# Kernel optimization log

Hardware: AMD Instinct MI355X
Metric: run time of the kernel (lower is better)

The kernel has to match this reference:

```python
import jax, jax.numpy as jnp
import numpy as np

POOLED_SIZES = [12, 16, 20, 24]
NUM_HEADS = 8
EPS_LN = 1e-5


def _pool_mat(in_size, out_size):
    # torch adaptive_avg_pool1d/2d semantics as an averaging matrix [out, in]
    m = np.zeros((out_size, in_size), np.float32)
    for i in range(out_size):
        s = (i * in_size) // out_size
        e = -((-(i + 1) * in_size) // out_size)  # ceil
        m[i, s:e] = 1.0 / (e - s)
    return jnp.asarray(m)


def _dwconv(x, w, b):
    # depthwise 3x3, stride 1, padding 1 (NCHW, OIHW with I=1)
    y = jax.lax.conv_general_dilated(
        x, w, (1, 1), 'SAME', feature_group_count=x.shape[1],
        dimension_numbers=('NCHW', 'OIHW', 'NCHW'))
    return y + b[None, :, None, None]


def _ln(x, g, b):
    m = x.mean(-1, keepdims=True)
    v = jnp.mean((x - m) ** 2, axis=-1, keepdims=True)
    return (x - m) / jnp.sqrt(v + EPS_LN) * g + b


def setup_inputs() -> dict:
    key = jax.random.key(0)
    ks = jax.random.split(key, 16)
    B, H, W, C = 4, 56, 56, 256
    hid = 4 * C
    nrm = lambda k, shape, s=0.02: jax.random.normal(k, shape, jnp.float32) * s
    inp = {
        'x': jax.random.normal(ks[0], (B, H * W, C), jnp.float32),
        'cpe_w': nrm(ks[1], (C, 1, 3, 3)), 'cpe_b': jnp.zeros((C,), jnp.float32),
        'norm1_w': jnp.ones((C,), jnp.float32), 'norm1_b': jnp.zeros((C,), jnp.float32),
        'q_w': nrm(ks[2], (C, C)),
        'kv_w': nrm(ks[3], (2 * C, C)),
        'attn_norm_w': jnp.ones((C,), jnp.float32), 'attn_norm_b': jnp.zeros((C,), jnp.float32),
        'proj_w': nrm(ks[4], (C, C)), 'proj_b': jnp.zeros((C,), jnp.float32),
        'norm2_w': jnp.ones((C,), jnp.float32), 'norm2_b': jnp.zeros((C,), jnp.float32),
        'fc1_w': nrm(ks[5], (hid, C)), 'fc1_b': jnp.zeros((hid,), jnp.float32),
        'irb_conv_w': nrm(ks[6], (hid, 1, 3, 3)), 'irb_conv_b': jnp.zeros((hid,), jnp.float32),
        'fc2_w': nrm(ks[7], (C, hid)), 'fc2_b': jnp.zeros((C,), jnp.float32),
        'H': H, 'W': W,
    }
    for i in range(4):
        inp[f'dconv{i}_w'] = nrm(ks[8 + i], (C, 1, 3, 3))
        inp[f'dconv{i}_b'] = jnp.zeros((C,), jnp.float32)
    return inp


def _forward(x, cpe_w, cpe_b, norm1_w, norm1_b, q_w, kv_w, attn_norm_w, attn_norm_b,
             proj_w, proj_b, dconv0_w, dconv0_b, dconv1_w, dconv1_b, dconv2_w, dconv2_b,
             dconv3_w, dconv3_b, norm2_w, norm2_b, fc1_w, fc1_b, irb_conv_w, irb_conv_b,
             fc2_w, fc2_b, H, W):
    B, N, C = x.shape
    nh = NUM_HEADS
    hd = C // nh
    scale = hd ** -0.5
    # conditional positional encoding: x = cpe(x) + x
    xi = x.transpose(0, 2, 1).reshape(B, C, H, W)
    xi = _dwconv(xi, cpe_w, cpe_b) + xi
    x = xi.reshape(B, C, N).transpose(0, 2, 1)
    # ---- pyramid pooling attention ----
    xn = _ln(x, norm1_w, norm1_b)
    q = (xn @ q_w.T).reshape(B, N, nh, hd).transpose(0, 2, 1, 3)  # [B,nh,N,hd]
    x_ = xn.transpose(0, 2, 1).reshape(B, C, H, W)
    dws = [(dconv0_w, dconv0_b), (dconv1_w, dconv1_b),
           (dconv2_w, dconv2_b), (dconv3_w, dconv3_b)]
    pools = []
    for p, (dw, db) in zip(POOLED_SIZES, dws):
        ph = _pool_mat(H, p)
        pw = _pool_mat(W, p)
        pool = jnp.einsum('oi,bcij,pj->bcop', ph, x_, pw)  # adaptive avg pool (p,p)
        pool = pool + _dwconv(pool, dw, db)
        pools.append(pool.reshape(B, C, -1))
    pools = jnp.concatenate(pools, axis=2).transpose(0, 2, 1)  # [B,P,C], P=1376
    pools = _ln(pools, attn_norm_w, attn_norm_b)
    kv = (pools @ kv_w.T).reshape(B, -1, 2, nh, hd).transpose(2, 0, 3, 1, 4)
    k, v = kv[0], kv[1]  # [B,nh,P,hd]
    attn = jax.nn.softmax(jnp.einsum('bhnd,bhpd->bhnp', q, k) * scale, axis=-1)
    out = jnp.einsum('bhnp,bhpd->bhnd', attn, v).transpose(0, 2, 1, 3).reshape(B, N, C)
    out = out @ proj_w.T + proj_b
    x = x + out
    # ---- IRB FFN ----
    xn = _ln(x, norm2_w, norm2_b)
    xi = xn.transpose(0, 2, 1).reshape(B, C, H, W)
    h = jnp.einsum('oc,bchw->bohw', fc1_w, xi) + fc1_b[None, :, None, None]
    h = jax.nn.gelu(h, approximate=False)
    h = h + _dwconv(h, irb_conv_w, irb_conv_b)
    o = jnp.einsum('oc,bchw->bohw', fc2_w, h) + fc2_b[None, :, None, None]
    x = x + o.reshape(B, C, N).transpose(0, 2, 1)
    return x


def reference(x, cpe_w, cpe_b, norm1_w, norm1_b, q_w, kv_w, attn_norm_w, attn_norm_b,
              proj_w, proj_b, dconv0_w, dconv0_b, dconv1_w, dconv1_b, dconv2_w, dconv2_b,
              dconv3_w, dconv3_b, norm2_w, norm2_b, fc1_w, fc1_b, irb_conv_w, irb_conv_b,
              fc2_w, fc2_b, H, W):
    return _forward(x, cpe_w, cpe_b, norm1_w, norm1_b, q_w, kv_w, attn_norm_w, attn_norm_b,
                    proj_w, proj_b, dconv0_w, dconv0_b, dconv1_w, dconv1_b, dconv2_w, dconv2_b,
                    dconv3_w, dconv3_b, norm2_w, norm2_b, fc1_w, fc1_b, irb_conv_w, irb_conv_b,
                    fc2_w, fc2_b, H, W)
```

## Files before the change

kernel.cpp:

```cpp
#include <hip/hip_runtime.h>
#include <hip/hip_bf16.h>

#define BQ 4
#define HH 56
#define WW 56
#define NN (HH*WW)
#define CC 256
#define NHEAD 8
#define HD 32
#define PP 1376
#define PPAD 1408
#define HIDN 1024
#define EPS_LN 1e-5f
#define QSCALE_LOG2E 0.25503484f

typedef unsigned short bf16u;
typedef __attribute__((ext_vector_type(8))) short short8;
typedef __attribute__((ext_vector_type(4))) float f32x4;

__device__ __forceinline__ float bf2f(bf16u u){
  union { unsigned int i; float f; } v; v.i = ((unsigned int)u) << 16; return v.f;
}
__device__ __forceinline__ bf16u f2bf(float f){
  unsigned int x = __float_as_uint(f);
  x += 0x7fffu + ((x >> 16) & 1u);
  return (bf16u)(x >> 16);
}
__device__ __forceinline__ bf16u f2bf_r(float f){
  return (bf16u)((__float_as_uint(f) + 0x8000u) >> 16);
}
__device__ __forceinline__ void cvt4(const ushort4 u, float* d){
  d[0]=bf2f(u.x); d[1]=bf2f(u.y); d[2]=bf2f(u.z); d[3]=bf2f(u.w);
}

#define CSEG 4
__global__ void k_init(const float* __restrict__ qw, const float* __restrict__ kvw,
                       const float* __restrict__ pw, const float* __restrict__ f1,
                       const float* __restrict__ f2, bf16u* __restrict__ wo,
                       const float* __restrict__ x, const float* __restrict__ w,
                       const float* __restrict__ bias, const float* __restrict__ g,
                       const float* __restrict__ be, float* __restrict__ x1,
                       bf16u* __restrict__ xnb){
  if (blockIdx.x < 768){
    int off = (blockIdx.x*256 + threadIdx.x) * 4;
    const float* s;
    if (off < 65536)       s = qw  + off;
    else if (off < 196608) s = kvw + off - 65536;
    else if (off < 262144) s = pw  + off - 196608;
    else if (off < 524288) s = f1  + off - 262144;
    else                   s = f2  + off - 524288;
    float4 v = *(const float4*)s;
    ushort4 u = {f2bf(v.x), f2bf(v.y), f2bf(v.z), f2bf(v.w)};
    *(ushort4*)(wo + off) = u;
    return;
  }
  int t = threadIdx.x;
  int wave = t >> 6, lane = t & 63;
  int widx = (blockIdx.x - 768)*4 + wave;
  const int nseg = WW/CSEG;
  int xseg = widx % nseg;
  int y    = (widx / nseg) % HH;
  int b    = widx / (nseg*HH);
  int c0 = lane*4;
  int x0 = xseg*CSEG;
  float wv[36];
  {
    const float* wp = w + (size_t)c0*9;
#pragma unroll
    for (int i = 0; i < 9; i++){
      float4 v = *(const float4*)(wp + i*4);
      wv[i*4+0]=v.x; wv[i*4+1]=v.y; wv[i*4+2]=v.z; wv[i*4+3]=v.w;
    }
  }
  float4 bi4 = *(const float4*)&bias[c0];
  float bi[4] = {bi4.x, bi4.y, bi4.z, bi4.w};
  float4 gv = *(const float4*)&g[c0];
  float4 bv = *(const float4*)&be[c0];
  const float* rowc = x + ((size_t)b*NN + (size_t)y*WW)*CC + c0;
  const float* rowm = (y > 0)    ? rowc - (size_t)WW*CC : rowc;
  const float* rowp = (y < HH-1) ? rowc + (size_t)WW*CC : rowc;
  if (y == 0){
#pragma unroll
    for (int cc = 0; cc < 4; cc++){ wv[cc*9+0]=0.f; wv[cc*9+1]=0.f; wv[cc*9+2]=0.f; }
  }
  if (y == HH-1){
#pragma unroll
    for (int cc = 0; cc < 4; cc++){ wv[cc*9+6]=0.f; wv[cc*9+7]=0.f; wv[cc*9+8]=0.f; }
  }
  float win[3][3][4];
  float4 rawA[3], rawB[3];
  if (x0 == 0){
#pragma unroll
    for (int r = 0; r < 3; r++)
#pragma unroll
      for (int cc = 0; cc < 4; cc++) win[0][r][cc] = 0.f;
  } else {
    size_t o = (size_t)(x0-1)*CC;
    float4 a0 = *(const float4*)&rowm[o];
    float4 a1 = *(const float4*)&rowc[o];
    float4 a2 = *(const float4*)&rowp[o];
    win[0][0][0]=a0.x; win[0][0][1]=a0.y; win[0][0][2]=a0.z; win[0][0][3]=a0.w;
    win[0][1][0]=a1.x; win[0][1][1]=a1.y; win[0][1][2]=a1.z; win[0][1][3]=a1.w;
    win[0][2][0]=a2.x; win[0][2][1]=a2.y; win[0][2][2]=a2.z; win[0][2][3]=a2.w;
  }
  {
    size_t o = (size_t)x0*CC;
    float4 a0 = *(const float4*)&rowm[o];
    float4 a1 = *(const float4*)&rowc[o];
    float4 a2 = *(const float4*)&rowp[o];
    win[1][0][0]=a0.x; win[1][0][1]=a0.y; win[1][0][2]=a0.z; win[1][0][3]=a0.w;
    win[1][1][0]=a1.x; win[1][1][1]=a1.y; win[1][1][2]=a1.z; win[1][1][3]=a1.w;
    win[1][2][0]=a2.x; win[1][2][1]=a2.y; win[1][2][2]=a2.z; win[1][2][3]=a2.w;
  }
  {
    size_t o = (size_t)(x0+1)*CC;
    rawA[0] = *(const float4*)&rowm[o];
    rawA[1] = *(const float4*)&rowc[o];
    rawA[2] = *(const float4*)&rowp[o];
  }
#pragma unroll
  for (int xx = 0; xx < CSEG; xx++){
    float4* cur = (xx & 1) ? rawB : rawA;
    float4* nxt = (xx & 1) ? rawA : rawB;
    if (xx < CSEG-1){
      int xg = x0 + xx + 2;
      if (xg < WW){
        size_t o = (size_t)xg*CC;
        nxt[0] = *(const float4*)&rowm[o];
        nxt[1] = *(const float4*)&rowc[o];
        nxt[2] = *(const float4*)&rowp[o];
      } else {
        float4 z = {0.f,0.f,0.f,0.f};
        nxt[0] = z; nxt[1] = z; nxt[2] = z;
      }
    }
    int sl2 = (xx+2)%3, slm = xx%3, slc = (xx+1)%3;
#pragma unroll
    for (int r = 0; r < 3; r++){
      win[sl2][r][0]=cur[r].x; win[sl2][r][1]=cur[r].y;
      win[sl2][r][2]=cur[r].z; win[sl2][r][3]=cur[r].w;
    }
    float o4[4];
#pragma unroll
    for (int cc = 0; cc < 4; cc++){
      float a = bi[cc];
      a += win[slm][0][cc]*wv[cc*9+0] + win[slc][0][cc]*wv[cc*9+1] + win[sl2][0][cc]*wv[cc*9+2];
      a += win[slm][1][cc]*wv[cc*9+3] + win[slc][1][cc]*wv[cc*9+4] + win[sl2][1][cc]*wv[cc*9+5];
      a += win[slm][2][cc]*wv[cc*9+6] + win[slc][2][cc]*wv[cc*9+7] + win[sl2][2][cc]*wv[cc*9+8];
      o4[cc] = win[slc][1][cc] + a;
    }
    size_t pix = (size_t)b*NN + (size_t)y*WW + x0 + xx;
    float4 ov = {o4[0],o4[1],o4[2],o4[3]};
    *(float4*)&x1[pix*CC + c0] = ov;
    float s  = o4[0]+o4[1]+o4[2]+o4[3];
    float s2 = o4[0]*o4[0]+o4[1]*o4[1]+o4[2]*o4[2]+o4[3]*o4[3];
#pragma unroll
    for (int off = 32; off; off >>= 1){
      s  += __shfl_xor(s,  off);
      s2 += __shfl_xor(s2, off);
    }
    float mean = s * (1.f/CC);
    float var  = s2 * (1.f/CC) - mean*mean;
    float rstd = rsqrtf(var + EPS_LN);
    float y0 = (o4[0]-mean)*rstd*gv.x + bv.x;
    float y1 = (o4[1]-mean)*rstd*gv.y + bv.y;
    float y2 = (o4[2]-mean)*rstd*gv.z + bv.z;
    float y3 = (o4[3]-mean)*rstd*gv.w + bv.w;
    ushort4 yb = {f2bf_r(y0), f2bf_r(y1), f2bf_r(y2), f2bf_r(y3)};
    *(ushort4*)&xnb[pix*CC + c0] = yb;
  }
}

__global__ void k_ln_bf16(const float* __restrict__ X, const float* __restrict__ g,
                          const float* __restrict__ be, bf16u* __restrict__ Y){
  int row = blockIdx.x;
  int t = threadIdx.x;
  float v = X[(size_t)row*CC + t];
  float s = v, s2 = v*v;
#pragma unroll
  for (int off = 32; off; off >>= 1){
    s  += __shfl_down(s,  off);
    s2 += __shfl_down(s2, off);
  }
  __shared__ float red[10];
  int wv_ = t >> 6, ln = t & 63;
  if (ln == 0){ red[wv_] = s; red[4+wv_] = s2; }
  __syncthreads();
  if (t == 0){
    float S  = red[0]+red[1]+red[2]+red[3];
    float S2 = red[4]+red[5]+red[6]+red[7];
    float mean = S * (1.f/CC);
    float var  = S2 * (1.f/CC) - mean*mean;
    red[8] = mean; red[9] = rsqrtf(var + EPS_LN);
  }
  __syncthreads();
  float mean = red[8], rstd = red[9];
  Y[(size_t)row*CC + t] = f2bf_r((v - mean) * rstd * g[t] + be[t]);
}

__global__ void k_pool(const bf16u* __restrict__ xnb, float* __restrict__ praw){
  int bp = blockIdx.x;
  int b = bp / PP, p = bp % PP;
  int ps, pi;
  if (p < 144)      { ps = 12; pi = p; }
  else if (p < 400) { ps = 16; pi = p - 144; }
  else if (p < 800) { ps = 20; pi = p - 400; }
  else              { ps = 24; pi = p - 800; }
  int oi = pi / ps, oj = pi % ps;
  int si = oi*HH/ps, ei = ((oi+1)*HH + ps - 1)/ps;
  int sj = oj*WW/ps, ej = ((oj+1)*WW + ps - 1)/ps;
  int c = threadIdx.x;
  const bf16u* xb = xnb + (size_t)b*NN*CC + c;
  float acc = 0.f;
  for (int i = si; i < ei; i++)
    for (int j = sj; j < ej; j++)
      acc += bf2f(xb[(size_t)(i*WW+j)*CC]);
  praw[(size_t)bp*CC + c] = acc / (float)((ei-si)*(ej-sj));
}

__global__ void k_pooldw_ln(const float* __restrict__ praw,
    const float* w0, const float* b0, const float* w1, const float* b1,
    const float* w2, const float* b2, const float* w3, const float* b3,
    const float* __restrict__ g, const float* __restrict__ be,
    bf16u* __restrict__ pools){
  int bp = blockIdx.x;
  int b = bp / PP, p = bp % PP;
  int ps, pi, off; const float *w, *bi;
  if (p < 144)      { ps=12; pi=p;     off=0;   w=w0; bi=b0; }
  else if (p < 400) { ps=16; pi=p-144; off=144; w=w1; bi=b1; }
  else if (p < 800) { ps=20; pi=p-400; off=400; w=w2; bi=b2; }
  else              { ps=24; pi=p-800; off=800; w=w3; bi=b3; }
  int oi = pi/ps, oj = pi%ps;
  int c = threadIdx.x;
  const float* base = praw + (size_t)(b*PP + off)*CC + c;
  float acc = bi[c];
#pragma unroll
  for (int kh = 0; kh < 3; kh++){
    int ii = oi + kh - 1; if (ii < 0 || ii >= ps) continue;
#pragma unroll
    for (int kw = 0; kw < 3; kw++){
      int jj = oj + kw - 1; if (jj < 0 || jj >= ps) continue;
      acc += base[(size_t)(ii*ps+jj)*CC] * w[c*9 + kh*3 + kw];
    }
  }
  float v = base[(size_t)(oi*ps+oj)*CC] + acc;
  float s = v, s2 = v*v;
#pragma unroll
  for (int o2_ = 32; o2_; o2_ >>= 1){
    s  += __shfl_down(s,  o2_);
    s2 += __shfl_down(s2, o2_);
  }
  __shared__ float red[10];
  int wv_ = c >> 6, ln = c & 63;
  if (ln == 0){ red[wv_] = s; red[4+wv_] = s2; }
  __syncthreads();
  if (c == 0){
    float S  = red[0]+red[1]+red[2]+red[3];
    float S2 = red[4]+red[5]+red[6]+red[7];
    float mean = S * (1.f/CC);
    float var  = S2 * (1.f/CC) - mean*mean;
    red[8] = mean; red[9] = rsqrtf(var + EPS_LN);
  }
  __syncthreads();
  float mean = red[8], rstd = red[9];
  pools[(size_t)bp*CC + c] = f2bf_r((v - mean) * rstd * g[c] + be[c]);
}

#define GST 40
template<int MT, int NT, bool OUT_BF16, bool HAS_BIAS, bool DO_GELU, bool HAS_RES, bool VT_OUT>
__global__ __launch_bounds__(256) void k_gemm_mfma(const bf16u* __restrict__ A,
                       const bf16u* __restrict__ Wt,
                       const float* __restrict__ bias, void* Outp,
                       const float* Res, bf16u* __restrict__ vtout,
                       int M, int Nout, int K, float oscale){
  constexpr int MW = (MT == 128) ? 4 : 2;
  constexpr int NW = (NT == 128) ? 4 : 2;
  __shared__ bf16u Ash[2][MT*GST];
  __shared__ bf16u Bsh[2][NT*GST];
  int t = threadIdx.x;
  int wave = t >> 6, lane = t & 63, quad = lane >> 4, l16 = lane & 15;
  int m0 = blockIdx.y * MT, n0 = blockIdx.x * NT;
  int wm = (wave >> 1) * (MT/2);
  int wn = (wave & 1) * (NT/2);
  int ar = (MT==128) ? (t>>1) : (t>>2);
  int ac = (MT==128) ? ((t&1)*16) : ((t&3)*8);
  int br = (NT==128) ? (t>>1) : (t>>2);
  int bc = (NT==128) ? ((t&1)*16) : ((t&3)*8);
  int astore = ar*GST + ac;
  int bstore = br*GST + bc;
  const bf16u* ap = A  + (size_t)(m0+ar)*K + ac;
  const bf16u* bp = Wt + (size_t)(n0+br)*K + bc;

  uint4 a0 = *(const uint4*)ap, a1;
  uint4 b0 = *(const uint4*)bp, b1;
  if constexpr (MT == 128) a1 = *(const uint4*)(ap+8);
  if constexpr (NT == 128) b1 = *(const uint4*)(bp+8);
  *(uint4*)&Ash[0][astore] = a0;
  if constexpr (MT == 128) *(uint4*)&Ash[0][astore + 8] = a1;
  *(uint4*)&Bsh[0][bstore] = b0;
  if constexpr (NT == 128) *(uint4*)&Bsh[0][bstore + 8] = b1;
  ap += 32; bp += 32;
  a0 = *(const uint4*)ap;
  if constexpr (MT == 128) a1 = *(const uint4*)(ap+8);
  b0 = *(const uint4*)bp;
  if constexpr (NT == 128) b1 = *(const uint4*)(bp+8);
  __syncthreads();

  f32x4 zero = {0.f,0.f,0.f,0.f};
  f32x4 acc[MW][NW];
#pragma unroll
  for (int i = 0; i < MW; i++)
#pragma unroll
    for (int j = 0; j < NW; j++) acc[i][j] = zero;

  int nks = K >> 5;
  for (int ks = 0; ks < nks; ks++){
    int cur = ks & 1;
    if (ks < nks-1){
      *(uint4*)&Ash[cur^1][astore] = a0;
      if constexpr (MT == 128) *(uint4*)&Ash[cur^1][astore + 8] = a1;
      *(uint4*)&Bsh[cur^1][bstore] = b0;
      if constexpr (NT == 128) *(uint4*)&Bsh[cur^1][bstore + 8] = b1;
      if (ks < nks-2){
        ap += 32; bp += 32;
        a0 = *(const uint4*)ap;
        if constexpr (MT == 128) a1 = *(const uint4*)(ap+8);
        b0 = *(const uint4*)bp;
        if constexpr (NT == 128) b1 = *(const uint4*)(bp+8);
      }
    }
    short8 af[MW], bfr[NW];
#pragma unroll
    for (int mi = 0; mi < MW; mi++)
      af[mi] = *(const short8*)&Ash[cur][(wm + mi*16 + l16)*GST + quad*8];
#pragma unroll
    for (int ni = 0; ni < NW; ni++)
      bfr[ni] = *(const short8*)&Bsh[cur][(wn + ni*16 + l16)*GST + quad*8];
#pragma unroll
    for (int mi = 0; mi < MW; mi++)
#pragma unroll
      for (int ni = 0; ni < NW; ni++)
        acc[mi][ni] = __builtin_amdgcn_mfma_f32_16x16x32_bf16(af[mi], bfr[ni], acc[mi][ni], 0,0,0);
    if (ks < nks-1) __syncthreads();
  }
#pragma unroll
  for (int mi = 0; mi < MW; mi++){
#pragma unroll
    for (int r = 0; r < 4; r++){
      int row = m0 + wm + mi*16 + quad*4 + r;
#pragma unroll
      for (int ni = 0; ni < NW; ni++){
        int col = n0 + wn + ni*16 + l16;
        float v = acc[mi][ni][r] * oscale;
        if constexpr (HAS_BIAS) v += bias[col];
        if constexpr (DO_GELU)  v = 0.5f*v*(1.f + erff(v*0.70710678118654752f));
        if constexpr (HAS_RES)  v += Res[(size_t)row*Nout + col];
        if constexpr (VT_OUT){
          if (col < CC){
            ((bf16u*)Outp)[(size_t)row*Nout + col] = f2bf_r(v);
          } else {
            int bb = row / PP, pp = row - bb*PP;
            vtout[((size_t)(bb*CC + (col - CC)))*PPAD + pp] = f2bf_r(v);
          }
        } else if constexpr (OUT_BF16){
          ((bf16u*)Outp)[(size_t)row*Nout + col] = f2bf_r(v);
        } else {
          ((float*)Outp)[(size_t)row*Nout + col] = v;
        }
      }
    }
  }
}

#define KST 40
#define VST 72
__global__ __launch_bounds__(256) void k_attn_mfma(const bf16u* __restrict__ q,
                       const bf16u* __restrict__ kvb, const bf16u* __restrict__ vt,
                       bf16u* __restrict__ out){
  __shared__ bf16u Ksh[2][64*KST];
  __shared__ bf16u Vsh[2][32*VST];
  int t = threadIdx.x;
  int wave = t >> 6, lane = t & 63, quad = lane >> 4, l16 = lane & 15;
  int bid = blockIdx.x;
  int qt = bid % (NN/64);
  int h  = (bid / (NN/64)) % NHEAD;
  int b  = bid / ((NN/64)*NHEAD);
  int q0 = qt*64 + wave*16;
  const bf16u* qptr = q + (size_t)(b*NN + q0 + l16)*CC + h*HD + quad*8;
  short8 qf = *(const short8*)qptr;
  f32x4 zero = {0.f,0.f,0.f,0.f};
  f32x4 o0 = zero, o1 = zero;
  float ls = 0.f;
  int ksr = t >> 2, ksc = (t & 3) * 8;
  int vsr = t >> 3, vsc = (t & 7) * 8;
  const bf16u* ksrc = kvb + (size_t)(b*PP + ksr)*(2*CC) + h*HD + ksc;
  const bf16u* vsrc = vt  + (size_t)(b*CC + h*HD + vsr)*PPAD + vsc;
  int krow = (ksr & 32) | ((ksr & 4) << 2) | ((ksr & 24) >> 1) | (ksr & 3);
  int kstore = krow*KST + ksc;
  int vstore = vsr*VST + vsc;
  int koffA = l16*KST + quad*8;
  int koffB = koffA + 16*KST;
  int voff0 = l16*VST + quad*8;
  int voff1 = (16 + l16)*VST + quad*8;

  uint4 kreg = *(const uint4*)ksrc;
  uint4 vreg = *(const uint4*)vsrc;
  *(uint4*)&Ksh[0][kstore] = kreg;
  *(uint4*)&Vsh[0][vstore] = vreg;
  ksrc += (size_t)64*(2*CC); vsrc += 64;
  kreg = *(const uint4*)ksrc; vreg = *(const uint4*)vsrc;
  __syncthreads();

#define PAIR(KB, VB, cb) { \
    short8 kfa = *(const short8*)&KB[cb*KST + koffA]; \
    short8 kfb = *(const short8*)&KB[cb*KST + koffB]; \
    f32x4 sa = __builtin_amdgcn_mfma_f32_16x16x32_bf16(kfa, qf, zero, 0,0,0); \
    f32x4 sb = __builtin_amdgcn_mfma_f32_16x16x32_bf16(kfb, qf, zero, 0,0,0); \
    float ea0 = __builtin_amdgcn_exp2f(sa[0]), ea1 = __builtin_amdgcn_exp2f(sa[1]); \
    float ea2 = __builtin_amdgcn_exp2f(sa[2]), ea3 = __builtin_amdgcn_exp2f(sa[3]); \
    float eb0 = __builtin_amdgcn_exp2f(sb[0]), eb1 = __builtin_amdgcn_exp2f(sb[1]); \
    float eb2 = __builtin_amdgcn_exp2f(sb[2]), eb3 = __builtin_amdgcn_exp2f(sb[3]); \
    ls += ((ea0+ea1)+(ea2+ea3)) + ((eb0+eb1)+(eb2+eb3)); \
    short8 pa; \
    pa[0]=(short)f2bf_r(ea0); pa[1]=(short)f2bf_r(ea1); \
    pa[2]=(short)f2bf_r(ea2); pa[3]=(short)f2bf_r(ea3); \
    pa[4]=(short)f2bf_r(eb0); pa[5]=(short)f2bf_r(eb1); \
    pa[6]=(short)f2bf_r(eb2); pa[7]=(short)f2bf_r(eb3); \
    short8 vf0 = *(const short8*)&VB[cb + voff0]; \
    short8 vf1 = *(const short8*)&VB[cb + voff1]; \
    o0 = __builtin_amdgcn_mfma_f32_16x16x32_bf16(pa, vf0, o0, 0,0,0); \
    o1 = __builtin_amdgcn_mfma_f32_16x16x32_bf16(pa, vf1, o1, 0,0,0); }

  for (int ch = 0; ch < PPAD/64 - 1; ch++){
    int cur = ch & 1;
    bf16u* KB = &Ksh[cur][0];
    bf16u* VB = &Vsh[cur][0];
    *(uint4*)&Ksh[cur^1][kstore] = kreg;
    *(uint4*)&Vsh[cur^1][vstore] = vreg;
    if (ch < PPAD/64 - 2){
      ksrc += (size_t)64*(2*CC); vsrc += 64;
      kreg = *(const uint4*)ksrc; vreg = *(const uint4*)vsrc;
    }
    PAIR(KB, VB, 0)
    PAIR(KB, VB, 32)
    __syncthreads();
  }
  {
    bf16u* KB = &Ksh[1][0];
    bf16u* VB = &Vsh[1][0];
    PAIR(KB, VB, 0)
  }
#undef PAIR

  ls += __shfl_xor(ls, 16); ls += __shfl_xor(ls, 32);
#pragma unroll
  for (int r = 0; r < 4; r++){
    int qq = quad*4 + r;
    float inv = 1.f / __shfl(ls, qq);
    size_t base = (size_t)(b*NN + q0 + qq)*CC + h*HD;
    out[base + l16]      = f2bf_r(o0[r]*inv);
    out[base + 16 + l16] = f2bf_r(o1[r]*inv);
  }
}

#define DWSEG 8
__global__ __launch_bounds__(256) void k_dwh(const bf16u* __restrict__ h, const float* __restrict__ w,
                      const float* __restrict__ bias, bf16u* __restrict__ h2){
  const int nseg = WW/DWSEG;
  int bid = blockIdx.x;
  int xseg = bid % nseg;
  int y    = (bid / nseg) % HH;
  int b    = bid / (nseg*HH);
  int t = threadIdx.x;
  int c0 = t*4;
  int x0 = xseg*DWSEG;
  float wv[36];
  {
    const float4* wp = (const float4*)(w + (size_t)c0*9);
#pragma unroll
    for (int i = 0; i < 9; i++){
      float4 v = wp[i];
      wv[i*4+0]=v.x; wv[i*4+1]=v.y; wv[i*4+2]=v.z; wv[i*4+3]=v.w;
    }
  }
  float4 bi4 = *(const float4*)&bias[c0];
  float bi[4] = {bi4.x, bi4.y, bi4.z, bi4.w};
  const bf16u* rowc = h + ((size_t)b*NN + (size_t)y*WW)*HIDN + c0;
  const bf16u* rowm = (y > 0)    ? rowc - (size_t)WW*HIDN : rowc;
  const bf16u* rowp = (y < HH-1) ? rowc + (size_t)WW*HIDN : rowc;
  if (y == 0){
#pragma unroll
    for (int cc = 0; cc < 4; cc++){ wv[cc*9+0]=0.f; wv[cc*9+1]=0.f; wv[cc*9+2]=0.f; }
  }
  if (y == HH-1){
#pragma unroll
    for (int cc = 0; cc < 4; cc++){ wv[cc*9+6]=0.f; wv[cc*9+7]=0.f; wv[cc*9+8]=0.f; }
  }
  float win[3][3][4];
  ushort4 rawA[3], rawB[3];
  if (x0 == 0){
#pragma unroll
    for (int r = 0; r < 3; r++)
#pragma unroll
      for (int cc = 0; cc < 4; cc++) win[0][r][cc] = 0.f;
  } else {
    size_t o = (size_t)(x0-1)*HIDN;
    ushort4 a0 = *(const ushort4*)&rowm[o];
    ushort4 a1 = *(const ushort4*)&rowc[o];
    ushort4 a2 = *(const ushort4*)&rowp[o];
    cvt4(a0, win[0][0]); cvt4(a1, win[0][1]); cvt4(a2, win[0][2]);
  }
  {
    size_t o = (size_t)x0*HIDN;
    ushort4 a0 = *(const ushort4*)&rowm[o];
    ushort4 a1 = *(const ushort4*)&rowc[o];
    ushort4 a2 = *(const ushort4*)&rowp[o];
    cvt4(a0, win[1][0]); cvt4(a1, win[1][1]); cvt4(a2, win[1][2]);
  }
  {
    size_t o = (size_t)(x0+1)*HIDN;
    rawA[0] = *(const ushort4*)&rowm[o];
    rawA[1] = *(const ushort4*)&rowc[o];
    rawA[2] = *(const ushort4*)&rowp[o];
  }
#pragma unroll
  for (int x = 0; x < DWSEG; x++){
    ushort4* cur = (x & 1) ? rawB : rawA;
    ushort4* nxt = (x & 1) ? rawA : rawB;
    if (x < DWSEG-1){
      int xg = x0 + x + 2;
      if (xg < WW){
        size_t o = (size_t)xg*HIDN;
        nxt[0] = *(const ushort4*)&rowm[o];
        nxt[1] = *(const ushort4*)&rowc[o];
        nxt[2] = *(const ushort4*)&rowp[o];
      } else {
        ushort4 z = {0,0,0,0};
        nxt[0] = z; nxt[1] = z; nxt[2] = z;
      }
    }
    int s2 = (x+2)%3, sm = x%3, sc_ = (x+1)%3;
    cvt4(cur[0], win[s2][0]); cvt4(cur[1], win[s2][1]); cvt4(cur[2], win[s2][2]);
    float o0[4];
#pragma unroll
    for (int cc = 0; cc < 4; cc++){
      float a = bi[cc];
      a += win[sm][0][cc]*wv[cc*9+0] + win[sc_][0][cc]*wv[cc*9+1] + win[s2][0][cc]*wv[cc*9+2];
      a += win[sm][1][cc]*wv[cc*9+3] + win[sc_][1][cc]*wv[cc*9+4] + win[s2][1][cc]*wv[cc*9+5];
      a += win[sm][2][cc]*wv[cc*9+6] + win[sc_][2][cc]*wv[cc*9+7] + win[s2][2][cc]*wv[cc*9+8];
      o0[cc] = win[sc_][1][cc] + a;
    }
    ushort4 ou = {f2bf_r(o0[0]), f2bf_r(o0[1]), f2bf_r(o0[2]), f2bf_r(o0[3])};
    *(ushort4*)&h2[((size_t)b*NN + (size_t)y*WW + x0 + x)*HIDN + c0] = ou;
  }
}

extern "C" void kernel_launch(void* const* d_in, const int* in_sizes, int n_in,
                              void* d_out, int out_size, void* d_ws, size_t ws_size,
                              hipStream_t stream){
  const float* x      = (const float*)d_in[0];
  const float* cpe_w  = (const float*)d_in[1];
  const float* cpe_b  = (const float*)d_in[2];
  const float* n1w    = (const float*)d_in[3];
  const float* n1b    = (const float*)d_in[4];
  const float* q_w    = (const float*)d_in[5];
  const float* kv_w   = (const float*)d_in[6];
  const float* anw    = (const float*)d_in[7];
  const float* anb    = (const float*)d_in[8];
  const float* proj_w = (const float*)d_in[9];
  const float* proj_b = (const float*)d_in[10];
  const float* n2w    = (const float*)d_in[11];
  const float* n2b    = (const float*)d_in[12];
  const float* fc1_w  = (const float*)d_in[13];
  const float* fc1_b  = (const float*)d_in[14];
  const float* irb_w  = (const float*)d_in[15];
  const float* irb_b  = (const float*)d_in[16];
  const float* fc2_w  = (const float*)d_in[17];
  const float* fc2_b  = (const float*)d_in[18];
  const float* dw0    = (const float*)d_in[21];
  const float* db0    = (const float*)d_in[22];
  const float* dw1    = (const float*)d_in[23];
  const float* db1    = (const float*)d_in[24];
  const float* dw2    = (const float*)d_in[25];
  const float* db2    = (const float*)d_in[26];
  const float* dw3    = (const float*)d_in[27];
  const float* db3    = (const float*)d_in[28];

  const size_t BNC = (size_t)BQ*NN*CC;
  const size_t BPC = (size_t)BQ*PP*CC;
  const size_t BNH = (size_t)BQ*NN*HIDN;

  float* x1   = (float*)d_ws;
  bf16u* xnb  = (bf16u*)(x1 + BNC);
  bf16u* wbuf = xnb + BNC;
  bf16u* wq   = wbuf;
  bf16u* wkv  = wbuf + 65536;
  bf16u* wpj  = wbuf + 196608;
  bf16u* wf1  = wbuf + 262144;
  bf16u* wf2  = wbuf + 524288;
  float* A0   = (float*)(wbuf + 786432);
  bf16u* qb   = (bf16u*)A0;
  float* praw = (float*)(qb + BNC);
  bf16u* poolsb = (bf16u*)(praw + BPC);
  bf16u* kvb  = poolsb + BPC;
  bf16u* vtb  = kvb + (size_t)BQ*PP*2*CC;
  bf16u* hbuf = (bf16u*)A0;
  bf16u* h2buf = hbuf + BNH;

  k_init<<<768 + (BQ*HH*(WW/CSEG))/4, 256, 0, stream>>>(q_w, kv_w, proj_w, fc1_w, fc2_w, wbuf,
                                            x, cpe_w, cpe_b, n1w, n1b, x1, xnb);
  k_gemm_mfma<64,64,true,false,false,false,false><<<dim3(CC/64, BQ*NN/64), 256, 0, stream>>>(
      xnb, wq, nullptr, qb, nullptr, nullptr, BQ*NN, CC, CC, QSCALE_LOG2E);
  k_pool<<<BQ*PP, 256, 0, stream>>>(xnb, praw);
  k_pooldw_ln<<<BQ*PP, 256, 0, stream>>>(praw, dw0,db0, dw1,db1, dw2,db2, dw3,db3,
                                         anw, anb, poolsb);
  k_gemm_mfma<64,64,true,false,false,false,true><<<dim3(2*CC/64, BQ*PP/64), 256, 0, stream>>>(
      poolsb, wkv, nullptr, kvb, nullptr, vtb, BQ*PP, 2*CC, CC, 1.0f);
  k_attn_mfma<<<BQ*NHEAD*(NN/64), 256, 0, stream>>>(qb, kvb, vtb, qb);
  k_gemm_mfma<64,64,false,true,false,true,false><<<dim3(CC/64, BQ*NN/64), 256, 0, stream>>>(
      qb, wpj, proj_b, x1, x1, nullptr, BQ*NN, CC, CC, 1.0f);
  k_ln_bf16<<<BQ*NN, 256, 0, stream>>>(x1, n2w, n2b, xnb);
  k_gemm_mfma<128,128,true,true,true,false,false><<<dim3(HIDN/128, BQ*NN/128), 256, 0, stream>>>(
      xnb, wf1, fc1_b, hbuf, nullptr, nullptr, BQ*NN, HIDN, CC, 1.0f);
  k_dwh<<<BQ*HH*(WW/DWSEG), 256, 0, stream>>>(hbuf, irb_w, irb_b, h2buf);
  k_gemm_mfma<64,64,false,true,false,true,false><<<dim3(CC/64, BQ*NN/64), 256, 0, stream>>>(
      h2buf, wf2, fc2_b, d_out, x1, nullptr, BQ*NN, CC, HIDN, 1.0f);
}
```

Baseline: 311.1 us.

## Deepen GEMM global prefetch, compute softmax sum via MFMA, warp-per-row LayerNorm

The GEMM main loop is unrolled by two and keeps two register sets of global prefetch, so loads are issued two K-steps ahead of use. In attention, the softmax denominator is now taken from an extra MFMA against a ones vector, which sums the bf16-rounded probabilities, and probabilities are packed with byte-perm instead of per-element conversion. The second LayerNorm now handles one row per wave using float4 loads and needs no shared-memory reduction or barriers. These changes cost more registers in the GEMM and one more MFMA per chunk in attention, and the normaliser now uses rounded rather than full-precision probabilities.

```diff
diff --git a/kernel.cpp b/kernel.cpp
--- a/kernel.cpp
+++ b/kernel.cpp
@@ -173,29 +173,27 @@
 
 __global__ void k_ln_bf16(const float* __restrict__ X, const float* __restrict__ g,
                           const float* __restrict__ be, bf16u* __restrict__ Y){
-  int row = blockIdx.x;
-  int t = threadIdx.x;
-  float v = X[(size_t)row*CC + t];
-  float s = v, s2 = v*v;
+  int wave = threadIdx.x >> 6, lane = threadIdx.x & 63;
+  int row = blockIdx.x*4 + wave;
+  int c0 = lane*4;
+  float4 v = *(const float4*)&X[(size_t)row*CC + c0];
+  float s  = v.x+v.y+v.z+v.w;
+  float s2 = v.x*v.x+v.y*v.y+v.z*v.z+v.w*v.w;
 #pragma unroll
   for (int off = 32; off; off >>= 1){
-    s  += __shfl_down(s,  off);
-    s2 += __shfl_down(s2, off);
-  }
-  __shared__ float red[10];
-  int wv_ = t >> 6, ln = t & 63;
-  if (ln == 0){ red[wv_] = s; red[4+wv_] = s2; }
-  __syncthreads();
-  if (t == 0){
-    float S  = red[0]+red[1]+red[2]+red[3];
-    float S2 = red[4]+red[5]+red[6]+red[7];
-    float mean = S * (1.f/CC);
-    float var  = S2 * (1.f/CC) - mean*mean;
-    red[8] = mean; red[9] = rsqrtf(var + EPS_LN);
-  }
-  __syncthreads();
-  float mean = red[8], rstd = red[9];
-  Y[(size_t)row*CC + t] = f2bf_r((v - mean) * rstd * g[t] + be[t]);
+    s  += __shfl_xor(s,  off);
+    s2 += __shfl_xor(s2, off);
+  }
+  float mean = s * (1.f/CC);
+  float var  = s2 * (1.f/CC) - mean*mean;
+  float rstd = rsqrtf(var + EPS_LN);
+  float4 gv = *(const float4*)&g[c0];
+  float4 bv = *(const float4*)&be[c0];
+  ushort4 yb = {f2bf_r((v.x-mean)*rstd*gv.x + bv.x),
+                f2bf_r((v.y-mean)*rstd*gv.y + bv.y),
+                f2bf_r((v.z-mean)*rstd*gv.z + bv.z),
+                f2bf_r((v.w-mean)*rstd*gv.w + bv.w)};
+  *(ushort4*)&Y[(size_t)row*CC + c0] = yb;
 }
 
 __global__ void k_pool(const bf16u* __restrict__ xnb, float* __restrict__ praw){
@@ -291,19 +289,27 @@
   const bf16u* ap = A  + (size_t)(m0+ar)*K + ac;
   const bf16u* bp = Wt + (size_t)(n0+br)*K + bc;
 
-  uint4 a0 = *(const uint4*)ap, a1;
-  uint4 b0 = *(const uint4*)bp, b1;
-  if constexpr (MT == 128) a1 = *(const uint4*)(ap+8);
-  if constexpr (NT == 128) b1 = *(const uint4*)(bp+8);
-  *(uint4*)&Ash[0][astore] = a0;
-  if constexpr (MT == 128) *(uint4*)&Ash[0][astore + 8] = a1;
-  *(uint4*)&Bsh[0][bstore] = b0;
-  if constexpr (NT == 128) *(uint4*)&Bsh[0][bstore + 8] = b1;
+  {
+    uint4 t0 = *(const uint4*)ap;
+    *(uint4*)&Ash[0][astore] = t0;
+    if constexpr (MT == 128){ uint4 t1 = *(const uint4*)(ap+8); *(uint4*)&Ash[0][astore+8] = t1; }
+    uint4 t2 = *(const uint4*)bp;
+    *(uint4*)&Bsh[0][bstore] = t2;
+    if constexpr (NT == 128){ uint4 t3 = *(const uint4*)(bp+8); *(uint4*)&Bsh[0][bstore+8] = t3; }
+  }
+  uint4 aA0, aA1, bA0, bA1;
+  uint4 aB0, aB1, bB0, bB1;
   ap += 32; bp += 32;
-  a0 = *(const uint4*)ap;
-  if constexpr (MT == 128) a1 = *(const uint4*)(ap+8);
-  b0 = *(const uint4*)bp;
-  if constexpr (NT == 128) b1 = *(const uint4*)(bp+8);
+  aA0 = *(const uint4*)ap;
+  if constexpr (MT == 128) aA1 = *(const uint4*)(ap+8);
+  bA0 = *(const uint4*)bp;
+  if constexpr (NT == 128) bA1 = *(const uint4*)(bp+8);
+  ap += 32; bp += 32;
+  aB0 = *(const uint4*)ap;
+  if constexpr (MT == 128) aB1 = *(const uint4*)(ap+8);
+  bB0 = *(const uint4*)bp;
+  if constexpr (NT == 128) bB1 = *(const uint4*)(bp+8);
+  ap += 32; bp += 32;
   __syncthreads();
 
   f32x4 zero = {0.f,0.f,0.f,0.f};
@@ -314,35 +320,57 @@
     for (int j = 0; j < NW; j++) acc[i][j] = zero;
 
   int nks = K >> 5;
-  for (int ks = 0; ks < nks; ks++){
-    int cur = ks & 1;
+
+#define GEMM_STEP(BUF) { \
+    short8 af[MW], bfr[NW]; \
+    _Pragma("unroll") \
+    for (int mi = 0; mi < MW; mi++) \
+      af[mi] = *(const short8*)&Ash[BUF][(wm + mi*16 + l16)*GST + quad*8]; \
+    _Pragma("unroll") \
+    for (int ni = 0; ni < NW; ni++) \
+      bfr[ni] = *(const short8*)&Bsh[BUF][(wn + ni*16 + l16)*GST + quad*8]; \
+    _Pragma("unroll") \
+    for (int mi = 0; mi < MW; mi++) \
+      _Pragma("unroll") \
+      for (int ni = 0; ni < NW; ni++) \
+        acc[mi][ni] = __builtin_amdgcn_mfma_f32_16x16x32_bf16(af[mi], bfr[ni], acc[mi][ni], 0,0,0); }
+
+  for (int ks = 0; ks < nks; ks += 2){
     if (ks < nks-1){
-      *(uint4*)&Ash[cur^1][astore] = a0;
-      if constexpr (MT == 128) *(uint4*)&Ash[cur^1][astore + 8] = a1;
-      *(uint4*)&Bsh[cur^1][bstore] = b0;
-      if constexpr (NT == 128) *(uint4*)&Bsh[cur^1][bstore + 8] = b1;
-      if (ks < nks-2){
+      *(uint4*)&Ash[1][astore] = aA0;
+      if constexpr (MT == 128) *(uint4*)&Ash[1][astore+8] = aA1;
+      *(uint4*)&Bsh[1][bstore] = bA0;
+      if constexpr (NT == 128) *(uint4*)&Bsh[1][bstore+8] = bA1;
+      if (ks < nks-3){
+        aA0 = *(const uint4*)ap;
+        if constexpr (MT == 128) aA1 = *(const uint4*)(ap+8);
+        bA0 = *(const uint4*)bp;
+        if constexpr (NT == 128) bA1 = *(const uint4*)(bp+8);
         ap += 32; bp += 32;
-        a0 = *(const uint4*)ap;
-        if constexpr (MT == 128) a1 = *(const uint4*)(ap+8);
-        b0 = *(const uint4*)bp;
-        if constexpr (NT == 128) b1 = *(const uint4*)(bp+8);
       }
     }
-    short8 af[MW], bfr[NW];
-#pragma unroll
-    for (int mi = 0; mi < MW; mi++)
-      af[mi] = *(const short8*)&Ash[cur][(wm + mi*16 + l16)*GST + quad*8];
-#pragma unroll
-    for (int ni = 0; ni < NW; ni++)
-      bfr[ni] = *(const short8*)&Bsh[cur][(wn + ni*16 + l16)*GST + quad*8];
-#pragma unroll
-    for (int mi = 0; mi < MW; mi++)
-#pragma unroll
-      for (int ni = 0; ni < NW; ni++)
-        acc[mi][ni] = __builtin_amdgcn_mfma_f32_16x16x32_bf16(af[mi], bfr[ni], acc[mi][ni], 0,0,0);
+    GEMM_STEP(0)
     if (ks < nks-1) __syncthreads();
-  }
+    if (ks+1 < nks-1){
+      *(uint4*)&Ash[0][astore] = aB0;
+      if constexpr (MT == 128) *(uint4*)&Ash[0][astore+8] = aB1;
+      *(uint4*)&Bsh[0][bstore] = bB0;
+      if constexpr (NT == 128) *(uint4*)&Bsh[0][bstore+8] = bB1;
+      if (ks+1 < nks-3){
+        aB0 = *(const uint4*)ap;
+        if constexpr (MT == 128) aB1 = *(const uint4*)(ap+8);
+        bB0 = *(const uint4*)bp;
+        if constexpr (NT == 128) bB1 = *(const uint4*)(bp+8);
+        ap += 32; bp += 32;
+      }
+    }
+    if (ks+1 < nks){
+      GEMM_STEP(1)
+      if (ks+1 < nks-1) __syncthreads();
+    }
+  }
+#undef GEMM_STEP
+
 #pragma unroll
   for (int mi = 0; mi < MW; mi++){
 #pragma unroll
@@ -389,8 +417,8 @@
   const bf16u* qptr = q + (size_t)(b*NN + q0 + l16)*CC + h*HD + quad*8;
   short8 qf = *(const short8*)qptr;
   f32x4 zero = {0.f,0.f,0.f,0.f};
-  f32x4 o0 = zero, o1 = zero;
-  float ls = 0.f;
+  f32x4 o0 = zero, o1 = zero, osum = zero;
+  const short8 onesf = {0x3F80,0x3F80,0x3F80,0x3F80,0x3F80,0x3F80,0x3F80,0x3F80};
   int ksr = t >> 2, ksc = (t & 3) * 8;
   int vsr = t >> 3, vsc = (t & 7) * 8;
   const bf16u* ksrc = kvb + (size_t)(b*PP + ksr)*(2*CC) + h*HD + ksc;
@@ -420,16 +448,21 @@
     float ea2 = __builtin_amdgcn_exp2f(sa[2]), ea3 = __builtin_amdgcn_exp2f(sa[3]); \
     float eb0 = __builtin_amdgcn_exp2f(sb[0]), eb1 = __builtin_amdgcn_exp2f(sb[1]); \
     float eb2 = __builtin_amdgcn_exp2f(sb[2]), eb3 = __builtin_amdgcn_exp2f(sb[3]); \
-    ls += ((ea0+ea1)+(ea2+ea3)) + ((eb0+eb1)+(eb2+eb3)); \
-    short8 pa; \
-    pa[0]=(short)f2bf_r(ea0); pa[1]=(short)f2bf_r(ea1); \
-    pa[2]=(short)f2bf_r(ea2); pa[3]=(short)f2bf_r(ea3); \
-    pa[4]=(short)f2bf_r(eb0); pa[5]=(short)f2bf_r(eb1); \
-    pa[6]=(short)f2bf_r(eb2); pa[7]=(short)f2bf_r(eb3); \
+    unsigned ra0 = __float_as_uint(ea0) + 0x8000u, ra1 = __float_as_uint(ea1) + 0x8000u; \
+    unsigned ra2 = __float_as_uint(ea2) + 0x8000u, ra3 = __float_as_uint(ea3) + 0x8000u; \
+    unsigned rb0 = __float_as_uint(eb0) + 0x8000u, rb1 = __float_as_uint(eb1) + 0x8000u; \
+    unsigned rb2 = __float_as_uint(eb2) + 0x8000u, rb3 = __float_as_uint(eb3) + 0x8000u; \
+    union { uint4 u; short8 s; } pk; \
+    pk.u.x = __builtin_amdgcn_perm(ra1, ra0, 0x07060302u); \
+    pk.u.y = __builtin_amdgcn_perm(ra3, ra2, 0x07060302u); \
+    pk.u.z = __builtin_amdgcn_perm(rb1, rb0, 0x07060302u); \
+    pk.u.w = __builtin_amdgcn_perm(rb3, rb2, 0x07060302u); \
+    short8 pa = pk.s; \
     short8 vf0 = *(const short8*)&VB[cb + voff0]; \
     short8 vf1 = *(const short8*)&VB[cb + voff1]; \
     o0 = __builtin_amdgcn_mfma_f32_16x16x32_bf16(pa, vf0, o0, 0,0,0); \
-    o1 = __builtin_amdgcn_mfma_f32_16x16x32_bf16(pa, vf1, o1, 0,0,0); }
+    o1 = __builtin_amdgcn_mfma_f32_16x16x32_bf16(pa, vf1, o1, 0,0,0); \
+    osum = __builtin_amdgcn_mfma_f32_16x16x32_bf16(pa, onesf, osum, 0,0,0); }
 
   for (int ch = 0; ch < PPAD/64 - 1; ch++){
     int cur = ch & 1;
@@ -452,11 +485,10 @@
   }
 #undef PAIR
 
-  ls += __shfl_xor(ls, 16); ls += __shfl_xor(ls, 32);
 #pragma unroll
   for (int r = 0; r < 4; r++){
     int qq = quad*4 + r;
-    float inv = 1.f / __shfl(ls, qq);
+    float inv = 1.f / osum[r];
     size_t base = (size_t)(b*NN + q0 + qq)*CC + h*HD;
     out[base + l16]      = f2bf_r(o0[r]*inv);
     out[base + 16 + l16] = f2bf_r(o1[r]*inv);
@@ -619,7 +651,7 @@
   k_attn_mfma<<<BQ*NHEAD*(NN/64), 256, 0, stream>>>(qb, kvb, vtb, qb);
   k_gemm_mfma<64,64,false,true,false,true,false><<<dim3(CC/64, BQ*NN/64), 256, 0, stream>>>(
       qb, wpj, proj_b, x1, x1, nullptr, BQ*NN, CC, CC, 1.0f);
-  k_ln_bf16<<<BQ*NN, 256, 0, stream>>>(x1, n2w, n2b, xnb);
+  k_ln_bf16<<<BQ*NN/4, 256, 0, stream>>>(x1, n2w, n2b, xnb);
   k_gemm_mfma<128,128,true,true,true,false,false><<<dim3(HIDN/128, BQ*NN/128), 256, 0, stream>>>(
       xnb, wf1, fc1_b, hbuf, nullptr, nullptr, BQ*NN, HIDN, CC, 1.0f);
   k_dwh<<<BQ*HH*(WW/DWSEG), 256, 0, stream>>>(hbuf, irb_w, irb_b, h2buf);
```

New measurement: 308.5 us. No clear change (-0.9%).
